# Optimization experiments

Hardware: AMD Instinct MI355X
Metric: run time of the kernel (lower is better)

The kernel has to match this reference:

```python
import jax, jax.numpy as jnp
import numpy as np

B, M, N, D = 16, 1024, 1024, 512
DIST_THRESH = 0.3
NUM_SINK = 8


def setup_inputs() -> dict:
    key = jax.random.key(0)
    k1, k2, k3, k4 = jax.random.split(key, 4)
    return {
        "tra_feats": jax.random.normal(k1, (B, M, D), jnp.float32),
        "det_feats": jax.random.normal(k2, (B, N, D), jnp.float32),
        "tra_loc": jax.random.uniform(k3, (B, M, 2), jnp.float32),
        "det_loc": jax.random.uniform(k4, (B, N, 2), jnp.float32),
        "alpha": jnp.ones((1,), jnp.float32),
        "eplison": jnp.zeros((1,), jnp.float32),
    }


def _sinkhorn(C, log_a, log_b, lambd, num_sink):
    # log-domain unrolled Sinkhorn: P_ij = exp(log_p), marginals a (rows), b (cols)
    log_p = -C / lambd
    def step(lp, _):
        lp = lp - (jax.nn.logsumexp(lp, axis=-1, keepdims=True) - log_a[:, None])
        lp = lp - (jax.nn.logsumexp(lp, axis=-2, keepdims=True) - log_b[None, :])
        return lp, None
    log_p, _ = jax.lax.scan(step, log_p, None, length=num_sink)
    # final row normalization (standard unrolled-sinkhorn convention)
    log_p = log_p - (jax.nn.logsumexp(log_p, axis=-1, keepdims=True) - log_a[:, None])
    return jnp.exp(log_p)


def _per_graph(tf, df, tl, dl, alpha, lambd):
    n1 = jnp.linalg.norm(tf, axis=-1, keepdims=True)          # [M,1]
    n2 = jnp.linalg.norm(df, axis=-1, keepdims=True)          # [N,1]
    d2 = jnp.sum((tl[:, None, :] - dl[None, :, :]) ** 2, -1)  # [M,N] squared cdist
    mask = (jnp.sqrt(d2) <= DIST_THRESH).astype(tf.dtype)
    corr = (tf @ df.T) / (n1 * n2.T) * mask                   # masked cosine similarity
    m, n = corr.shape
    # augment with dustbin row/col filled with learnable alpha
    top = jnp.concatenate([corr, jnp.full((m, 1), alpha, corr.dtype)], axis=1)
    bot = jnp.full((1, n + 1), alpha, corr.dtype)
    couplings = jnp.concatenate([top, bot], axis=0)           # [M+1, N+1]
    norm = 1.0 / (m + n)
    a_aug = jnp.full((m + 1,), norm, corr.dtype).at[-1].set(norm * n)
    b_aug = jnp.full((n + 1,), norm, corr.dtype).at[-1].set(norm * m)
    p = _sinkhorn(1.0 - couplings, jnp.log(a_aug), jnp.log(b_aug), lambd, NUM_SINK)
    return p * (m + n)


def reference(tra_feats, det_feats, tra_loc, det_loc, alpha, eplison):
    a = alpha[0]
    lambd = jnp.exp(eplison[0]) + 0.03
    f = jax.vmap(lambda tf, df, tl, dl: _per_graph(tf, df, tl, dl, a, lambd))
    return f(tra_feats, det_feats, tra_loc, det_loc)   # [B, M+1, N+1]
```

## Files before the change

### kernel.cpp

```cpp
#include <hip/hip_runtime.h>
#include <math.h>

#define B_ 16
#define M_ 1024
#define N_ 1024
#define D_ 512
#define MP1 1025
#define NP1 1025
#define NUM_SINK 8
#define BK 64
#define SSTR 1024
#define VSTR 1028
#define NCHK 16
#define LOG_NORM (-7.6246189861593985f)
#define LOG_HALF (-0.6931471805599453f)

typedef __attribute__((ext_vector_type(8))) short bf16x8;
typedef __attribute__((ext_vector_type(4))) float f32x4;
typedef __attribute__((ext_vector_type(8))) _Float16 h16x8;

__device__ inline short f2bf(float x) {
    unsigned u = __builtin_bit_cast(unsigned, x);
    u = (u + 0x7FFFu + ((u >> 16) & 1u)) >> 16;
    return (short)u;
}

__device__ inline void gload16(const void* g, void* l) {
    __builtin_amdgcn_global_load_lds(
        (const __attribute__((address_space(1))) unsigned int*)g,
        (__attribute__((address_space(3))) unsigned int*)l, 16, 0, 0);
}

template<bool PRE>
__global__ __launch_bounds__(256) void norms_kernel_t(
    const float* __restrict__ tf, const float* __restrict__ df,
    float* __restrict__ inv1, float* __restrict__ inv2,
    unsigned short* __restrict__ tfh, unsigned short* __restrict__ dfh,
    float* __restrict__ v, float* __restrict__ sums_p)
{
    if (PRE && blockIdx.x == 0) {
        const int nv = B_ * VSTR, ns = 2 * B_ * 17;
        for (int t = threadIdx.x; t < nv + ns; t += 256) {
            if (t < nv) v[t] = 0.f;
            else {
                int u2 = t - nv;
                int p = u2 / (B_ * 17), s = u2 % 17;
                sums_p[u2] = (p == 0 && s == 0) ? 1025.0f : 0.f;
            }
        }
    }
    int w = (blockIdx.x * 256 + threadIdx.x) >> 6;
    int lane = threadIdx.x & 63;
    if (w >= B_ * 2048) return;
    int b = w >> 11;
    int rr = w & 2047;
    const float* src;
    float* dst = nullptr;
    unsigned short* dsth = nullptr;
    if (rr < M_) { src = tf + ((size_t)b * M_ + rr) * D_;
                   if (!PRE) dst = inv1 + b * M_ + rr;
                   if (PRE)  dsth = tfh + ((size_t)b * M_ + rr) * D_; }
    else         { src = df + ((size_t)b * N_ + (rr - M_)) * D_;
                   if (!PRE) dst = inv2 + b * N_ + (rr - M_);
                   if (PRE)  dsth = dfh + ((size_t)b * N_ + (rr - M_)) * D_; }
    float4 x = *(const float4*)(src + lane * 4);
    float4 y = *(const float4*)(src + 256 + lane * 4);
    float ss = x.x*x.x + x.y*x.y + x.z*x.z + x.w*x.w
             + y.x*y.x + y.y*y.y + y.z*y.z + y.w*y.w;
    #pragma unroll
    for (int o = 32; o; o >>= 1) ss += __shfl_xor(ss, o);
    if (PRE) {
        float rn = rsqrtf(ss);
        ushort4 hx, hy;
        hx.x = (unsigned short)f2bf(x.x*rn); hx.y = (unsigned short)f2bf(x.y*rn);
        hx.z = (unsigned short)f2bf(x.z*rn); hx.w = (unsigned short)f2bf(x.w*rn);
        hy.x = (unsigned short)f2bf(y.x*rn); hy.y = (unsigned short)f2bf(y.y*rn);
        hy.z = (unsigned short)f2bf(y.z*rn); hy.w = (unsigned short)f2bf(y.w*rn);
        *(ushort4*)(dsth + lane * 4) = hx;
        *(ushort4*)(dsth + 256 + lane * 4) = hy;
    } else {
        if (lane == 0) *dst = 1.0f / sqrtf(ss);
    }
}

template<int MODE>
__global__ __launch_bounds__(256) void gemm_s_kernel(
    const void* __restrict__ A, const void* __restrict__ Bm,
    const float* __restrict__ tl, const float* __restrict__ dl,
    const float* __restrict__ inv1, const float* __restrict__ inv2,
    const float* __restrict__ eps_p, void* __restrict__ Sout)
{
    __shared__ __align__(16) unsigned short As[2][128 * BK];
    __shared__ __align__(16) unsigned short Bs[2][128 * BK];

    int flat = blockIdx.x;
    int swz = (flat & 7) * 128 + (flat >> 3);
    int jb = swz & 7, ib = (swz >> 3) & 7;
    int b  = swz >> 6;
    int i0 = ib * 128;
    int j0 = jb * 128;

    int tid  = threadIdx.x;
    int lane = tid & 63;
    int w    = tid >> 6;
    int wm   = w >> 1, wn = w & 1;

    f32x4 acc[4][4] = {};

    if constexpr (MODE == 2) {
        const unsigned short* Ah = (const unsigned short*)A  + (size_t)b * M_ * D_;
        const unsigned short* Bh = (const unsigned short*)Bm + (size_t)b * N_ * D_;
        int gcol = ((lane & 7) ^ (lane >> 3)) << 3;
        int rloc = lane >> 3;

        auto stage = [&](int k0, int buf) {
            #pragma unroll
            for (int c = 0; c < 4; ++c) {
                int r = (w * 4 + c) * 8 + rloc;
                gload16(Ah + (size_t)(i0 + r) * D_ + k0 + gcol,
                        (char*)As[buf] + (w * 4 + c) * 1024 + lane * 16);
                gload16(Bh + (size_t)(j0 + r) * D_ + k0 + gcol,
                        (char*)Bs[buf] + (w * 4 + c) * 1024 + lane * 16);
            }
        };

        stage(0, 0);
        __syncthreads();
        int cur = 0;
        for (int t = 0; t < D_ / BK; ++t) {
            if (t < D_ / BK - 1) stage((t + 1) * BK, cur ^ 1);
            #pragma unroll
            for (int ks = 0; ks < 2; ++ks) {
                int kb = ks * 64 + ((lane >> 4) << 4);
                bf16x8 af[4], bfr[4];
                #pragma unroll
                for (int m = 0; m < 4; ++m) {
                    int ra = wm * 64 + m * 16 + (lane & 15);
                    af[m] = *(const bf16x8*)((const char*)As[cur] + ra * 128 + (kb ^ ((ra & 7) << 4)));
                    int rb = wn * 64 + m * 16 + (lane & 15);
                    bfr[m] = *(const bf16x8*)((const char*)Bs[cur] + rb * 128 + (kb ^ ((rb & 7) << 4)));
                }
                #pragma unroll
                for (int m = 0; m < 4; ++m)
                    #pragma unroll
                    for (int n = 0; n < 4; ++n)
                        acc[m][n] = __builtin_amdgcn_mfma_f32_16x16x32_bf16(af[m], bfr[n], acc[m][n], 0, 0, 0);
            }
            __syncthreads();
            cur ^= 1;
        }
    } else {
        const float* Ab = (const float*)A  + (size_t)b * M_ * D_;
        const float* Bb = (const float*)Bm + (size_t)b * N_ * D_;
        int seg   = tid & 7;
        int rbase = tid >> 3;
        for (int k0 = 0; k0 < D_; k0 += BK) {
            #pragma unroll
            for (int rr = 0; rr < 4; ++rr) {
                int r = rbase + rr * 32;
                int colx = (seg * 16) ^ ((r & 7) << 4);
                {
                    const float* pa = Ab + (size_t)(i0 + r) * D_ + k0 + seg * 8;
                    float4 a0 = *(const float4*)pa;
                    float4 a1 = *(const float4*)(pa + 4);
                    bf16x8 hv;
                    hv[0] = f2bf(a0.x); hv[1] = f2bf(a0.y); hv[2] = f2bf(a0.z); hv[3] = f2bf(a0.w);
                    hv[4] = f2bf(a1.x); hv[5] = f2bf(a1.y); hv[6] = f2bf(a1.z); hv[7] = f2bf(a1.w);
                    *(bf16x8*)((char*)As[0] + r * 128 + colx) = hv;
                }
                {
                    const float* pb = Bb + (size_t)(j0 + r) * D_ + k0 + seg * 8;
                    float4 b0 = *(const float4*)pb;
                    float4 b1 = *(const float4*)(pb + 4);
                    bf16x8 hv;
                    hv[0] = f2bf(b0.x); hv[1] = f2bf(b0.y); hv[2] = f2bf(b0.z); hv[3] = f2bf(b0.w);
                    hv[4] = f2bf(b1.x); hv[5] = f2bf(b1.y); hv[6] = f2bf(b1.z); hv[7] = f2bf(b1.w);
                    *(bf16x8*)((char*)Bs[0] + r * 128 + colx) = hv;
                }
            }
            __syncthreads();
            #pragma unroll
            for (int ks = 0; ks < 2; ++ks) {
                int kb = ks * 64 + ((lane >> 4) << 4);
                bf16x8 af[4], bfr[4];
                #pragma unroll
                for (int m = 0; m < 4; ++m) {
                    int ra = wm * 64 + m * 16 + (lane & 15);
                    af[m] = *(const bf16x8*)((const char*)As[0] + ra * 128 + (kb ^ ((ra & 7) << 4)));
                    int rb = wn * 64 + m * 16 + (lane & 15);
                    bfr[m] = *(const bf16x8*)((const char*)Bs[0] + rb * 128 + (kb ^ ((rb & 7) << 4)));
                }
                #pragma unroll
                for (int m = 0; m < 4; ++m)
                    #pragma unroll
                    for (int n = 0; n < 4; ++n)
                        acc[m][n] = __builtin_amdgcn_mfma_f32_16x16x32_bf16(af[m], bfr[n], acc[m][n], 0, 0, 0);
            }
            __syncthreads();
        }
    }

    float lam = __expf(eps_p[0]) + 0.03f;
    float inv_lam = 1.0f / lam;
    int crow0 = i0 + wm * 64;
    int ccol0 = j0 + wn * 64;
    int rlane = lane >> 4;
    int clane = lane & 15;

    float invb_[4], dlx_[4], dly_[4];
    #pragma unroll
    for (int n = 0; n < 4; ++n) {
        int j = ccol0 + n * 16 + clane;
        if (MODE != 2) invb_[n] = inv2[b * N_ + j];
        dlx_[n]  = dl[((size_t)b * N_ + j) * 2 + 0];
        dly_[n]  = dl[((size_t)b * N_ + j) * 2 + 1];
    }
    #pragma unroll
    for (int m = 0; m < 4; ++m) {
        #pragma unroll
        for (int reg = 0; reg < 4; ++reg) {
            int i = crow0 + m * 16 + rlane * 4 + reg;
            float inva = (MODE != 2) ? inv1[b * M_ + i] : 1.0f;
            float tlx  = tl[((size_t)b * M_ + i) * 2 + 0];
            float tly  = tl[((size_t)b * M_ + i) * 2 + 1];
            #pragma unroll
            for (int n = 0; n < 4; ++n) {
                float cosv = (MODE == 2) ? acc[m][n][reg]
                                         : acc[m][n][reg] * inva * invb_[n];
                float dx = tlx - dlx_[n];
                float dy = tly - dly_[n];
                float mi = (fmaf(dx, dx, dy * dy) <= 0.09f) ? inv_lam : 0.0f;
                float val = fmaf(cosv, mi, -inv_lam);
                int col = ccol0 + n * 16 + clane;
                if (MODE >= 1) {
                    _Float16* Srow = (_Float16*)Sout + ((size_t)b * M_ + i) * SSTR;
                    Srow[col] = (_Float16)val;
                } else {
                    float* Srow = (float*)Sout + ((size_t)b * MP1 + i) * NP1;
                    Srow[col] = val;
                }
            }
        }
    }
}

__global__ __launch_bounds__(256) void init_hv(
    float* __restrict__ v, float* __restrict__ sums_p)
{
    int t = blockIdx.x * 256 + threadIdx.x;
    if (t < B_ * VSTR) v[t] = 0.f;
    int u2 = t - B_ * VSTR;
    if (u2 >= 0 && u2 < 2 * B_ * 17) {
        int p = u2 / (B_ * 17), s = u2 % 17;
        sums_p[u2] = (p == 0 && s == 0) ? 1025.0f : 0.f;
    }
}

__global__ __launch_bounds__(256, 1) void rowcol64(
    const _Float16* __restrict__ Sh, const float* __restrict__ v,
    float* __restrict__ ps,
    const float* __restrict__ alpha_p, const float* __restrict__ eps_p)
{
    int blk = blockIdx.x;
    int b = blk >> 4, k = blk & 15;
    int tid = threadIdx.x, lane = tid & 63, w = tid >> 6;

    __shared__ float red[4][64][17];

    const float* vb = v + (size_t)b * VSTR;
    float vreg[16];
    {
        float4 v0 = *(const float4*)(vb + lane * 8);
        float4 v1 = *(const float4*)(vb + lane * 8 + 4);
        float4 v2 = *(const float4*)(vb + 512 + lane * 8);
        float4 v3 = *(const float4*)(vb + 512 + lane * 8 + 4);
        vreg[0]=v0.x; vreg[1]=v0.y; vreg[2]=v0.z; vreg[3]=v0.w;
        vreg[4]=v1.x; vreg[5]=v1.y; vreg[6]=v1.z; vreg[7]=v1.w;
        vreg[8]=v2.x; vreg[9]=v2.y; vreg[10]=v2.z; vreg[11]=v2.w;
        vreg[12]=v3.x; vreg[13]=v3.y; vreg[14]=v3.z; vreg[15]=v3.w;
    }
    float lam = __expf(eps_p[0]) + 0.03f;
    float s_a = (alpha_p[0] - 1.0f) / lam;
    float et16c = __expf(s_a + vb[1024]);

    const _Float16* Sb = Sh + ((size_t)b << 20);
    int rbase = k * 64 + w * 16;

    h16x8 h0[16], h1[16];
    #pragma unroll
    for (int rr = 0; rr < 16; ++rr) {
        const _Float16* row = Sb + (size_t)(rbase + rr) * SSTR;
        h0[rr] = *(const h16x8*)(row + lane * 8);
        h1[rr] = *(const h16x8*)(row + 512 + lane * 8);
    }

    float creg[16] = {};
    float sum_scale = 0.f;

    #pragma unroll
    for (int rr = 0; rr < 16; ++rr) {
        float et[16];
        float rs = 0.f;
        #pragma unroll
        for (int e = 0; e < 8; ++e) { et[e] = __expf((float)h0[rr][e] + vreg[e]); rs += et[e]; }
        #pragma unroll
        for (int e = 0; e < 8; ++e) { et[8+e] = __expf((float)h1[rr][e] + vreg[8+e]); rs += et[8+e]; }
        #pragma unroll
        for (int o = 32; o; o >>= 1) rs += __shfl_xor(rs, o);
        rs += et16c;
        float scale = (1.0f / 2048.0f) / rs;
        #pragma unroll
        for (int e = 0; e < 16; ++e) creg[e] += et[e] * scale;
        sum_scale += scale;
    }

    #pragma unroll
    for (int e = 0; e < 16; ++e) red[w][lane][e] = creg[e];
    if (lane == 0) red[w][0][16] = sum_scale;
    __syncthreads();

    float* pso = ps + (size_t)(k * 16 + b) * 1025;
    for (int j = tid; j < 1024; j += 256) {
        int lane_j = (j & 511) >> 3;
        int e_j    = ((j >> 9) << 3) | (j & 7);
        pso[j] = red[0][lane_j][e_j] + red[1][lane_j][e_j]
               + red[2][lane_j][e_j] + red[3][lane_j][e_j];
    }
    if (tid == 0)
        pso[1024] = et16c * (red[0][0][16] + red[1][0][16] + red[2][0][16] + red[3][0][16]);
}

__global__ __launch_bounds__(256) void colpass32(
    const float* __restrict__ ps, float* __restrict__ v,
    float* __restrict__ sums_p, int it)
{
    int gw = blockIdx.x * 4 + (threadIdx.x >> 6);
    int lane = threadIdx.x & 63;
    if (gw >= B_ * 17) return;
    int b = gw / 17, seg = gw % 17;
    int j = seg * 64 + lane;
    int par = it & 1;
    float sum_old = 0.f;
    #pragma unroll
    for (int s = 0; s < 17; ++s) sum_old += sums_p[par * (B_ * 17) + b * 17 + s];
    float ev = 0.f;
    if (j <= 1024) {
        size_t vidx = (size_t)b * VSTR + j;
        float vj = v[vidx];
        const float* pp = ps + (size_t)b * 1025 + j;
        float cs = 0.f;
        #pragma unroll
        for (int c = 0; c < NCHK; ++c) cs += pp[(size_t)c * (16 * 1025)];
        cs += 0.5f * __expf(vj) / sum_old;
        float lb = (j == 1024) ? LOG_HALF : LOG_NORM;
        float vn = vj + lb - __logf(cs);
        v[vidx] = vn;
        ev = __expf(vn);
    }
    #pragma unroll
    for (int o = 32; o; o >>= 1) ev += __shfl_xor(ev, o);
    if (lane == 0) sums_p[(par ^ 1) * (B_ * 17) + b * 17 + seg] = ev;
}

__global__ __launch_bounds__(256) void final32(
    const _Float16* __restrict__ Sh, const float* __restrict__ v,
    const float* __restrict__ sums_p,
    const float* __restrict__ alpha_p, const float* __restrict__ eps_p,
    float* __restrict__ out)
{
    int blk = blockIdx.x;
    int tid = threadIdx.x, lane = tid & 63, w = tid >> 6;

    if (blk >= 512) {
        int gw = (blk - 512) * 4 + w;
        if (gw >= B_ * 17) return;
        int b = gw / 17, seg = gw % 17, j = seg * 64 + lane;
        if (j > 1024) return;
        float sumv = 0.f;
        int par = NUM_SINK & 1;
        #pragma unroll
        for (int s = 0; s < 17; ++s) sumv += sums_p[par * (B_ * 17) + b * 17 + s];
        out[((size_t)b * MP1 + 1024) * NP1 + j] = __expf(v[(size_t)b * VSTR + j]) * 1024.0f / sumv;
        return;
    }

    int b = blk >> 5, k = blk & 31;
    const float* vb = v + (size_t)b * VSTR;
    float vreg[16];
    {
        float4 v0 = *(const float4*)(vb + lane * 8);
        float4 v1 = *(const float4*)(vb + lane * 8 + 4);
        float4 v2 = *(const float4*)(vb + 512 + lane * 8);
        float4 v3 = *(const float4*)(vb + 512 + lane * 8 + 4);
        vreg[0]=v0.x; vreg[1]=v0.y; vreg[2]=v0.z; vreg[3]=v0.w;
        vreg[4]=v1.x; vreg[5]=v1.y; vreg[6]=v1.z; vreg[7]=v1.w;
        vreg[8]=v2.x; vreg[9]=v2.y; vreg[10]=v2.z; vreg[11]=v2.w;
        vreg[12]=v3.x; vreg[13]=v3.y; vreg[14]=v3.z; vreg[15]=v3.w;
    }
    float lam = __expf(eps_p[0]) + 0.03f;
    float s_a = (alpha_p[0] - 1.0f) / lam;
    float et16c = __expf(s_a + vb[1024]);

    const _Float16* Sb = Sh + ((size_t)b << 20);
    int rbase = k * 32 + w * 8;

    #pragma unroll
    for (int g = 0; g < 2; ++g) {
        h16x8 h0[4], h1[4];
        #pragma unroll
        for (int rr = 0; rr < 4; ++rr) {
            const _Float16* row = Sb + (size_t)(rbase + g * 4 + rr) * SSTR;
            h0[rr] = *(const h16x8*)(row + lane * 8);
            h1[rr] = *(const h16x8*)(row + 512 + lane * 8);
        }
        #pragma unroll
        for (int rr = 0; rr < 4; ++rr) {
            int r = rbase + g * 4 + rr;
            float et[16];
            float rs = 0.f;
            #pragma unroll
            for (int e = 0; e < 8; ++e) { et[e] = __expf((float)h0[rr][e] + vreg[e]); rs += et[e]; }
            #pragma unroll
            for (int e = 0; e < 8; ++e) { et[8+e] = __expf((float)h1[rr][e] + vreg[8+e]); rs += et[8+e]; }
            #pragma unroll
            for (int o = 32; o; o >>= 1) rs += __shfl_xor(rs, o);
            rs += et16c;
            float sc = 1.0f / rs;
            float* orow = out + ((size_t)b * MP1 + r) * NP1;
            float4 o0 = {et[0]*sc,  et[1]*sc,  et[2]*sc,  et[3]*sc};
            float4 o1 = {et[4]*sc,  et[5]*sc,  et[6]*sc,  et[7]*sc};
            float4 o2 = {et[8]*sc,  et[9]*sc,  et[10]*sc, et[11]*sc};
            float4 o3 = {et[12]*sc, et[13]*sc, et[14]*sc, et[15]*sc};
            *(float4*)(orow + lane * 8)           = o0;
            *(float4*)(orow + lane * 8 + 4)       = o1;
            *(float4*)(orow + 512 + lane * 8)     = o2;
            *(float4*)(orow + 512 + lane * 8 + 4) = o3;
            if (lane == 0) orow[1024] = et16c * sc;
        }
    }
}


__global__ __launch_bounds__(256) void fill_edges_f32(
    float* __restrict__ Sout, const float* __restrict__ alpha_p, const float* __restrict__ eps_p)
{
    int t = blockIdx.x * 256 + threadIdx.x;
    if (t >= B_ * (NP1 + M_)) return;
    int b = t / (NP1 + M_), r = t % (NP1 + M_);
    float lam = expf(eps_p[0]) + 0.03f;
    float s = (alpha_p[0] - 1.0f) / lam;
    size_t idx;
    if (r < NP1) idx = ((size_t)b * MP1 + M_) * NP1 + r;
    else         idx = ((size_t)b * MP1 + (r - NP1)) * NP1 + N_;
    Sout[idx] = s;
}

__global__ __launch_bounds__(256) void row_pass_kernel(
    const float* __restrict__ S, const float* __restrict__ v, float* __restrict__ u)
{
    int w = (blockIdx.x * 256 + threadIdx.x) >> 6;
    int lane = threadIdx.x & 63;
    if (w >= B_ * MP1) return;
    int b = w / MP1, i = w % MP1;
    const float* row = S + ((size_t)b * MP1 + i) * NP1;
    const float* vb = v + b * NP1;
    float sm = 0.f;
    #pragma unroll
    for (int q = 0; q < 17; ++q) {
        int j = lane + q * 64;
        if (j < NP1) sm += expf(row[j] + vb[j]);
    }
    #pragma unroll
    for (int o = 32; o; o >>= 1) sm += __shfl_xor(sm, o);
    if (lane == 0) {
        float la = (i == M_) ? LOG_HALF : LOG_NORM;
        u[b * MP1 + i] = la - logf(sm);
    }
}

__global__ __launch_bounds__(256) void col_pass1_kernel(
    const float* __restrict__ S, const float* __restrict__ u,
    float* __restrict__ pm, float* __restrict__ ps)
{
    int j = blockIdx.x * 256 + threadIdx.x;
    int b = blockIdx.z;
    int i0 = blockIdx.y * 128;
    int i1 = min(i0 + 128, MP1);
    if (j >= NP1) return;
    const float* p  = S + ((size_t)b * MP1 + i0) * NP1 + j;
    const float* ub = u + b * MP1;
    float sm = 0.f;
    for (int i = i0; i < i1; ++i) {
        sm += expf(*p + ub[i]);
        p += NP1;
    }
    int idx = (blockIdx.y * B_ + b) * NP1 + j;
    pm[idx] = 0.f;
    ps[idx] = sm;
}

__global__ __launch_bounds__(256) void col_pass2_kernel(
    const float* __restrict__ pm, const float* __restrict__ ps, float* __restrict__ v)
{
    int j = blockIdx.x * 256 + threadIdx.x;
    int b = blockIdx.y;
    if (j >= NP1) return;
    float Ssum = 0.f;
    #pragma unroll
    for (int c = 0; c < 9; ++c) Ssum += ps[(c * B_ + b) * NP1 + j];
    float lb = (j == N_) ? LOG_HALF : LOG_NORM;
    v[b * NP1 + j] = lb - logf(Ssum);
}

__global__ __launch_bounds__(256) void row_final_kernel(
    float* __restrict__ S, const float* __restrict__ v)
{
    int w = (blockIdx.x * 256 + threadIdx.x) >> 6;
    int lane = threadIdx.x & 63;
    if (w >= B_ * MP1) return;
    int b = w / MP1, i = w % MP1;
    float* row = S + ((size_t)b * MP1 + i) * NP1;
    const float* vb = v + b * NP1;
    float et[17];
    float sm = 0.f;
    #pragma unroll
    for (int q = 0; q < 17; ++q) {
        int j = lane + q * 64;
        float e = 0.f;
        if (j < NP1) e = expf(row[j] + vb[j]);
        et[q] = e;
        sm += e;
    }
    #pragma unroll
    for (int o = 32; o; o >>= 1) sm += __shfl_xor(sm, o);
    float A = (i == M_) ? 0.5f : (1.0f / 2048.0f);
    float scale = (A / sm) * 2048.0f;
    #pragma unroll
    for (int q = 0; q < 17; ++q) {
        int j = lane + q * 64;
        if (j < NP1) row[j] = et[q] * scale;
    }
}

__global__ __launch_bounds__(256) void zero_kernel(float* __restrict__ p, int n)
{
    int i = blockIdx.x * 256 + threadIdx.x;
    if (i < n) p[i] = 0.f;
}

extern "C" void kernel_launch(void* const* d_in, const int* in_sizes, int n_in,
                              void* d_out, int out_size, void* d_ws, size_t ws_size,
                              hipStream_t stream)
{
    const float* tf    = (const float*)d_in[0];
    const float* df    = (const float*)d_in[1];
    const float* tl    = (const float*)d_in[2];
    const float* dl    = (const float*)d_in[3];
    const float* alpha = (const float*)d_in[4];
    const float* eps   = (const float*)d_in[5];
    float* out = (float*)d_out;

    const size_t bf_one   = (size_t)B_ * M_ * D_ * 2;
    const size_t sh_bytes = (size_t)B_ * M_ * SSTR * 2;
    const size_t vf       = (size_t)B_ * VSTR;
    const size_t sums_f   = 2 * B_ * 17;
    const size_t invs_f   = (size_t)B_ * M_ * 2;
    const size_t need_pre = 2 * bf_one + sh_bytes + (vf + sums_f) * 4 + 512;
    const size_t need_mid = sh_bytes + (vf + sums_f + invs_f) * 4 + 512;

    int initblocks = (int)((vf + sums_f + 255) / 256);

    if (ws_size >= need_pre) {
        unsigned short* tfh = (unsigned short*)d_ws;
        unsigned short* dfh = tfh + (size_t)B_ * M_ * D_;
        _Float16* Sh = (_Float16*)((char*)d_ws + 2 * bf_one);
        float* fbase = (float*)((char*)d_ws + ((2 * bf_one + sh_bytes + 255) & ~(size_t)255));
        float* v      = fbase;
        float* sums_p = v + vf;
        float* ps     = out;

        norms_kernel_t<true><<<(B_ * 2048) / 4, 256, 0, stream>>>(tf, df, nullptr, nullptr, tfh, dfh, v, sums_p);
        gemm_s_kernel<2><<<1024, 256, 0, stream>>>(tfh, dfh, tl, dl, nullptr, nullptr, eps, Sh);

        for (int it = 0; it < NUM_SINK; ++it) {
            rowcol64<<<256, 256, 0, stream>>>(Sh, v, ps, alpha, eps);
            colpass32<<<68, 256, 0, stream>>>(ps, v, sums_p, it);
        }
        final32<<<580, 256, 0, stream>>>(Sh, v, sums_p, alpha, eps, out);
    } else if (ws_size >= need_mid) {
        _Float16* Sh = (_Float16*)d_ws;
        float* fbase = (float*)((char*)d_ws + ((sh_bytes + 255) & ~(size_t)255));
        float* inv1   = fbase;
        float* inv2   = inv1 + B_ * M_;
        float* v      = inv2 + B_ * N_;
        float* sums_p = v + vf;
        float* ps     = out;

        init_hv<<<initblocks, 256, 0, stream>>>(v, sums_p);
        norms_kernel_t<false><<<(B_ * 2048) / 4, 256, 0, stream>>>(tf, df, inv1, inv2, nullptr, nullptr, nullptr, nullptr);
        gemm_s_kernel<1><<<1024, 256, 0, stream>>>(tf, df, tl, dl, inv1, inv2, eps, Sh);

        for (int it = 0; it < NUM_SINK; ++it) {
            rowcol64<<<256, 256, 0, stream>>>(Sh, v, ps, alpha, eps);
            colpass32<<<68, 256, 0, stream>>>(ps, v, sums_p, it);
        }
        final32<<<580, 256, 0, stream>>>(Sh, v, sums_p, alpha, eps, out);
    } else {
        float* S = out;
        float* ws = (float*)d_ws;
        float* inv1 = ws;
        float* inv2 = inv1 + B_ * M_;
        float* u    = inv2 + B_ * N_;
        float* v    = u + B_ * MP1;
        float* pm   = v + B_ * NP1;
        float* ps   = pm + 9 * B_ * NP1;

        zero_kernel<<<(B_ * NP1 + 255) / 256, 256, 0, stream>>>(v, B_ * NP1);
        norms_kernel_t<false><<<(B_ * 2048) / 4, 256, 0, stream>>>(tf, df, inv1, inv2, nullptr, nullptr, nullptr, nullptr);
        gemm_s_kernel<0><<<1024, 256, 0, stream>>>(tf, df, tl, dl, inv1, inv2, eps, S);
        fill_edges_f32<<<(B_ * (NP1 + M_) + 255) / 256, 256, 0, stream>>>(S, alpha, eps);

        int rowblocks = (B_ * MP1 + 3) / 4;
        for (int it = 0; it < NUM_SINK; ++it) {
            row_pass_kernel<<<rowblocks, 256, 0, stream>>>(S, v, u);
            col_pass1_kernel<<<dim3(5, 9, 16), 256, 0, stream>>>(S, u, pm, ps);
            col_pass2_kernel<<<dim3(5, 16), 256, 0, stream>>>(pm, ps, v);
        }
        row_final_kernel<<<rowblocks, 256, 0, stream>>>(S, v);
    }
}
```

Before: 150.9 us.

## Fuse column-update pass into row kernel with ping-pong v and partial-sum buffers

Removes the separate colpass32 launch per Sinkhorn iteration. Each rowcolv64 block now recomputes the column potential v for its batch redundantly from the previous iteration's partial sums, using double-buffered v and ps arrays indexed by iteration parity. Initialisation of v is handled by an it==0 branch instead of a separate init step. The aim is to cut 8 launches and their inter-kernel gaps. The cost is redundant per-block column reductions (16 blocks per batch each read 16x1025 partials) and a larger workspace.

New measurement: 168.8 us. 11.9% more time.

```diff
diff --git a/kernel.cpp b/kernel.cpp
--- a/kernel.cpp
+++ b/kernel.cpp
@@ -12,6 +12,7 @@
 #define SSTR 1024
 #define VSTR 1028
 #define NCHK 16
+#define PSTOT (16 * B_ * 1025)
 #define LOG_NORM (-7.6246189861593985f)
 #define LOG_HALF (-0.6931471805599453f)
 
@@ -35,20 +36,8 @@
 __global__ __launch_bounds__(256) void norms_kernel_t(
     const float* __restrict__ tf, const float* __restrict__ df,
     float* __restrict__ inv1, float* __restrict__ inv2,
-    unsigned short* __restrict__ tfh, unsigned short* __restrict__ dfh,
-    float* __restrict__ v, float* __restrict__ sums_p)
-{
-    if (PRE && blockIdx.x == 0) {
-        const int nv = B_ * VSTR, ns = 2 * B_ * 17;
-        for (int t = threadIdx.x; t < nv + ns; t += 256) {
-            if (t < nv) v[t] = 0.f;
-            else {
-                int u2 = t - nv;
-                int p = u2 / (B_ * 17), s = u2 % 17;
-                sums_p[u2] = (p == 0 && s == 0) ? 1025.0f : 0.f;
-            }
-        }
-    }
+    unsigned short* __restrict__ tfh, unsigned short* __restrict__ dfh)
+{
     int w = (blockIdx.x * 256 + threadIdx.x) >> 6;
     int lane = threadIdx.x & 63;
     if (w >= B_ * 2048) return;
@@ -244,44 +233,19 @@
     }
 }
 
-__global__ __launch_bounds__(256) void init_hv(
-    float* __restrict__ v, float* __restrict__ sums_p)
-{
-    int t = blockIdx.x * 256 + threadIdx.x;
-    if (t < B_ * VSTR) v[t] = 0.f;
-    int u2 = t - B_ * VSTR;
-    if (u2 >= 0 && u2 < 2 * B_ * 17) {
-        int p = u2 / (B_ * 17), s = u2 % 17;
-        sums_p[u2] = (p == 0 && s == 0) ? 1025.0f : 0.f;
-    }
-}
-
-__global__ __launch_bounds__(256, 1) void rowcol64(
-    const _Float16* __restrict__ Sh, const float* __restrict__ v,
-    float* __restrict__ ps,
-    const float* __restrict__ alpha_p, const float* __restrict__ eps_p)
+__global__ __launch_bounds__(256, 1) void rowcolv64(
+    const _Float16* __restrict__ Sh, float* __restrict__ vbuf,
+    float* __restrict__ psbuf,
+    const float* __restrict__ alpha_p, const float* __restrict__ eps_p,
+    int it)
 {
     int blk = blockIdx.x;
     int b = blk >> 4, k = blk & 15;
     int tid = threadIdx.x, lane = tid & 63, w = tid >> 6;
 
     __shared__ float red[4][64][17];
-
-    const float* vb = v + (size_t)b * VSTR;
-    float vreg[16];
-    {
-        float4 v0 = *(const float4*)(vb + lane * 8);
-        float4 v1 = *(const float4*)(vb + lane * 8 + 4);
-        float4 v2 = *(const float4*)(vb + 512 + lane * 8);
-        float4 v3 = *(const float4*)(vb + 512 + lane * 8 + 4);
-        vreg[0]=v0.x; vreg[1]=v0.y; vreg[2]=v0.z; vreg[3]=v0.w;
-        vreg[4]=v1.x; vreg[5]=v1.y; vreg[6]=v1.z; vreg[7]=v1.w;
-        vreg[8]=v2.x; vreg[9]=v2.y; vreg[10]=v2.z; vreg[11]=v2.w;
-        vreg[12]=v3.x; vreg[13]=v3.y; vreg[14]=v3.z; vreg[15]=v3.w;
-    }
-    float lam = __expf(eps_p[0]) + 0.03f;
-    float s_a = (alpha_p[0] - 1.0f) / lam;
-    float et16c = __expf(s_a + vb[1024]);
+    __shared__ float vsh[1025];
+    __shared__ float wred[4];
 
     const _Float16* Sb = Sh + ((size_t)b << 20);
     int rbase = k * 64 + w * 16;
@@ -294,6 +258,57 @@
         h1[rr] = *(const h16x8*)(row + 512 + lane * 8);
     }
 
+    int rp = it & 1, wp = rp ^ 1;
+
+    if (it == 0) {
+        for (int j = tid; j < 1025; j += 256) vsh[j] = 0.f;
+    } else {
+        const float* vin = vbuf + (size_t)rp * (B_ * VSTR) + (size_t)b * VSTR;
+        const float* pin = psbuf + (size_t)rp * PSTOT + (size_t)b * 1025;
+        float vp[4]; float vp4 = 0.f;
+        float evs = 0.f;
+        #pragma unroll
+        for (int q = 0; q < 4; ++q) { vp[q] = vin[tid + q * 256]; evs += __expf(vp[q]); }
+        if (tid == 0) { vp4 = vin[1024]; evs += __expf(vp4); }
+        #pragma unroll
+        for (int o = 32; o; o >>= 1) evs += __shfl_xor(evs, o);
+        if (lane == 0) wred[w] = evs;
+        __syncthreads();
+        float Sev = wred[0] + wred[1] + wred[2] + wred[3];
+        #pragma unroll
+        for (int q = 0; q < 4; ++q) {
+            int j = tid + q * 256;
+            float cs = 0.f;
+            #pragma unroll
+            for (int c = 0; c < NCHK; ++c) cs += pin[(size_t)c * (B_ * 1025) + j];
+            cs += 0.5f * __expf(vp[q]) / Sev;
+            vsh[j] = vp[q] + LOG_NORM - __logf(cs);
+        }
+        if (tid == 0) {
+            float cs = 0.f;
+            #pragma unroll
+            for (int c = 0; c < NCHK; ++c) cs += pin[(size_t)c * (B_ * 1025) + 1024];
+            cs += 0.5f * __expf(vp4) / Sev;
+            vsh[1024] = vp4 + LOG_HALF - __logf(cs);
+        }
+    }
+    __syncthreads();
+
+    if (k == 0) {
+        float* vout = vbuf + (size_t)wp * (B_ * VSTR) + (size_t)b * VSTR;
+        for (int j = tid; j < 1025; j += 256) vout[j] = vsh[j];
+    }
+
+    float vreg[16];
+    #pragma unroll
+    for (int e = 0; e < 8; ++e) {
+        vreg[e]     = vsh[lane * 8 + e];
+        vreg[8 + e] = vsh[512 + lane * 8 + e];
+    }
+    float lam = __expf(eps_p[0]) + 0.03f;
+    float s_a = (alpha_p[0] - 1.0f) / lam;
+    float et16c = __expf(s_a + vsh[1024]);
+
     float creg[16] = {};
     float sum_scale = 0.f;
 
@@ -319,7 +334,7 @@
     if (lane == 0) red[w][0][16] = sum_scale;
     __syncthreads();
 
-    float* pso = ps + (size_t)(k * 16 + b) * 1025;
+    float* pso = psbuf + (size_t)wp * PSTOT + (size_t)(k * B_ + b) * 1025;
     for (int j = tid; j < 1024; j += 256) {
         int lane_j = (j & 511) >> 3;
         int e_j    = ((j >> 9) << 3) | (j & 7);
@@ -330,76 +345,77 @@
         pso[1024] = et16c * (red[0][0][16] + red[1][0][16] + red[2][0][16] + red[3][0][16]);
 }
 
-__global__ __launch_bounds__(256) void colpass32(
-    const float* __restrict__ ps, float* __restrict__ v,
-    float* __restrict__ sums_p, int it)
-{
-    int gw = blockIdx.x * 4 + (threadIdx.x >> 6);
-    int lane = threadIdx.x & 63;
-    if (gw >= B_ * 17) return;
-    int b = gw / 17, seg = gw % 17;
-    int j = seg * 64 + lane;
-    int par = it & 1;
-    float sum_old = 0.f;
-    #pragma unroll
-    for (int s = 0; s < 17; ++s) sum_old += sums_p[par * (B_ * 17) + b * 17 + s];
-    float ev = 0.f;
-    if (j <= 1024) {
-        size_t vidx = (size_t)b * VSTR + j;
-        float vj = v[vidx];
-        const float* pp = ps + (size_t)b * 1025 + j;
-        float cs = 0.f;
-        #pragma unroll
-        for (int c = 0; c < NCHK; ++c) cs += pp[(size_t)c * (16 * 1025)];
-        cs += 0.5f * __expf(vj) / sum_old;
-        float lb = (j == 1024) ? LOG_HALF : LOG_NORM;
-        float vn = vj + lb - __logf(cs);
-        v[vidx] = vn;
-        ev = __expf(vn);
-    }
-    #pragma unroll
-    for (int o = 32; o; o >>= 1) ev += __shfl_xor(ev, o);
-    if (lane == 0) sums_p[(par ^ 1) * (B_ * 17) + b * 17 + seg] = ev;
-}
-
-__global__ __launch_bounds__(256) void final32(
-    const _Float16* __restrict__ Sh, const float* __restrict__ v,
-    const float* __restrict__ sums_p,
+__global__ __launch_bounds__(256) void finalv(
+    const _Float16* __restrict__ Sh, const float* __restrict__ vbuf,
+    const float* __restrict__ psbuf,
     const float* __restrict__ alpha_p, const float* __restrict__ eps_p,
     float* __restrict__ out)
 {
     int blk = blockIdx.x;
+    bool dust = blk >= 512;
+    int b = dust ? (blk - 512) : (blk >> 5);
+    int k = blk & 31;
     int tid = threadIdx.x, lane = tid & 63, w = tid >> 6;
 
-    if (blk >= 512) {
-        int gw = (blk - 512) * 4 + w;
-        if (gw >= B_ * 17) return;
-        int b = gw / 17, seg = gw % 17, j = seg * 64 + lane;
-        if (j > 1024) return;
-        float sumv = 0.f;
-        int par = NUM_SINK & 1;
-        #pragma unroll
-        for (int s = 0; s < 17; ++s) sumv += sums_p[par * (B_ * 17) + b * 17 + s];
-        out[((size_t)b * MP1 + 1024) * NP1 + j] = __expf(v[(size_t)b * VSTR + j]) * 1024.0f / sumv;
+    __shared__ float vsh[1025];
+    __shared__ float wred[4];
+
+    const int rp = NUM_SINK & 1;
+    {
+        const float* vin = vbuf + (size_t)rp * (B_ * VSTR) + (size_t)b * VSTR;
+        const float* pin = psbuf + (size_t)rp * PSTOT + (size_t)b * 1025;
+        float vp[4]; float vp4 = 0.f;
+        float evs = 0.f;
+        #pragma unroll
+        for (int q = 0; q < 4; ++q) { vp[q] = vin[tid + q * 256]; evs += __expf(vp[q]); }
+        if (tid == 0) { vp4 = vin[1024]; evs += __expf(vp4); }
+        #pragma unroll
+        for (int o = 32; o; o >>= 1) evs += __shfl_xor(evs, o);
+        if (lane == 0) wred[w] = evs;
+        __syncthreads();
+        float Sev = wred[0] + wred[1] + wred[2] + wred[3];
+        #pragma unroll
+        for (int q = 0; q < 4; ++q) {
+            int j = tid + q * 256;
+            float cs = 0.f;
+            #pragma unroll
+            for (int c = 0; c < NCHK; ++c) cs += pin[(size_t)c * (B_ * 1025) + j];
+            cs += 0.5f * __expf(vp[q]) / Sev;
+            vsh[j] = vp[q] + LOG_NORM - __logf(cs);
+        }
+        if (tid == 0) {
+            float cs = 0.f;
+            #pragma unroll
+            for (int c = 0; c < NCHK; ++c) cs += pin[(size_t)c * (B_ * 1025) + 1024];
+            cs += 0.5f * __expf(vp4) / Sev;
+            vsh[1024] = vp4 + LOG_HALF - __logf(cs);
+        }
+    }
+    __syncthreads();
+
+    if (dust) {
+        float evs = 0.f;
+        for (int j = tid; j < 1025; j += 256) evs += __expf(vsh[j]);
+        #pragma unroll
+        for (int o = 32; o; o >>= 1) evs += __shfl_xor(evs, o);
+        if (lane == 0) wred[w] = evs;
+        __syncthreads();
+        float Sev8 = wred[0] + wred[1] + wred[2] + wred[3];
+        float* orow = out + ((size_t)b * MP1 + 1024) * NP1;
+        for (int j = tid; j < 1025; j += 256)
+            orow[j] = __expf(vsh[j]) * 1024.0f / Sev8;
         return;
     }
 
-    int b = blk >> 5, k = blk & 31;
-    const float* vb = v + (size_t)b * VSTR;
     float vreg[16];
-    {
-        float4 v0 = *(const float4*)(vb + lane * 8);
-        float4 v1 = *(const float4*)(vb + lane * 8 + 4);
-        float4 v2 = *(const float4*)(vb + 512 + lane * 8);
-        float4 v3 = *(const float4*)(vb + 512 + lane * 8 + 4);
-        vreg[0]=v0.x; vreg[1]=v0.y; vreg[2]=v0.z; vreg[3]=v0.w;
-        vreg[4]=v1.x; vreg[5]=v1.y; vreg[6]=v1.z; vreg[7]=v1.w;
-        vreg[8]=v2.x; vreg[9]=v2.y; vreg[10]=v2.z; vreg[11]=v2.w;
-        vreg[12]=v3.x; vreg[13]=v3.y; vreg[14]=v3.z; vreg[15]=v3.w;
+    #pragma unroll
+    for (int e = 0; e < 8; ++e) {
+        vreg[e]     = vsh[lane * 8 + e];
+        vreg[8 + e] = vsh[512 + lane * 8 + e];
     }
     float lam = __expf(eps_p[0]) + 0.03f;
     float s_a = (alpha_p[0] - 1.0f) / lam;
-    float et16c = __expf(s_a + vb[1024]);
+    float et16c = __expf(s_a + vsh[1024]);
 
     const _Float16* Sb = Sh + ((size_t)b << 20);
     int rbase = k * 32 + w * 8;
@@ -562,49 +578,40 @@
 
     const size_t bf_one   = (size_t)B_ * M_ * D_ * 2;
     const size_t sh_bytes = (size_t)B_ * M_ * SSTR * 2;
-    const size_t vf       = (size_t)B_ * VSTR;
-    const size_t sums_f   = 2 * B_ * 17;
+    const size_t vf2      = 2 * (size_t)B_ * VSTR;
+    const size_t ps2      = 2 * (size_t)PSTOT;
     const size_t invs_f   = (size_t)B_ * M_ * 2;
-    const size_t need_pre = 2 * bf_one + sh_bytes + (vf + sums_f) * 4 + 512;
-    const size_t need_mid = sh_bytes + (vf + sums_f + invs_f) * 4 + 512;
-
-    int initblocks = (int)((vf + sums_f + 255) / 256);
+    const size_t need_pre = 2 * bf_one + sh_bytes + (vf2 + ps2) * 4 + 512;
+    const size_t need_mid = sh_bytes + (vf2 + ps2 + invs_f) * 4 + 512;
 
     if (ws_size >= need_pre) {
         unsigned short* tfh = (unsigned short*)d_ws;
         unsigned short* dfh = tfh + (size_t)B_ * M_ * D_;
         _Float16* Sh = (_Float16*)((char*)d_ws + 2 * bf_one);
         float* fbase = (float*)((char*)d_ws + ((2 * bf_one + sh_bytes + 255) & ~(size_t)255));
-        float* v      = fbase;
-        float* sums_p = v + vf;
-        float* ps     = out;
-
-        norms_kernel_t<true><<<(B_ * 2048) / 4, 256, 0, stream>>>(tf, df, nullptr, nullptr, tfh, dfh, v, sums_p);
+        float* vbuf  = fbase;
+        float* psbuf = vbuf + vf2;
+
+        norms_kernel_t<true><<<(B_ * 2048) / 4, 256, 0, stream>>>(tf, df, nullptr, nullptr, tfh, dfh);
         gemm_s_kernel<2><<<1024, 256, 0, stream>>>(tfh, dfh, tl, dl, nullptr, nullptr, eps, Sh);
 
-        for (int it = 0; it < NUM_SINK; ++it) {
-            rowcol64<<<256, 256, 0, stream>>>(Sh, v, ps, alpha, eps);
-            colpass32<<<68, 256, 0, stream>>>(ps, v, sums_p, it);
-        }
-        final32<<<580, 256, 0, stream>>>(Sh, v, sums_p, alpha, eps, out);
+        for (int it = 0; it < NUM_SINK; ++it)
+            rowcolv64<<<256, 256, 0, stream>>>(Sh, vbuf, psbuf, alpha, eps, it);
+        finalv<<<512 + B_, 256, 0, stream>>>(Sh, vbuf, psbuf, alpha, eps, out);
     } else if (ws_size >= need_mid) {
         _Float16* Sh = (_Float16*)d_ws;
         float* fbase = (float*)((char*)d_ws + ((sh_bytes + 255) & ~(size_t)255));
-        float* inv1   = fbase;
-        float* inv2   = inv1 + B_ * M_;
-        float* v      = inv2 + B_ * N_;
-        float* sums_p = v + vf;
-        float* ps     = out;
-
-        init_hv<<<initblocks, 256, 0, stream>>>(v, sums_p);
-        norms_kernel_t<false><<<(B_ * 2048) / 4, 256, 0, stream>>>(tf, df, inv1, inv2, nullptr, nullptr, nullptr, nullptr);
+        float* inv1  = fbase;
+        float* inv2  = inv1 + B_ * M_;
+        float* vbuf  = inv2 + B_ * N_;
+        float* psbuf = vbuf + vf2;
+
+        norms_kernel_t<false><<<(B_ * 2048) / 4, 256, 0, stream>>>(tf, df, inv1, inv2, nullptr, nullptr);
         gemm_s_kernel<1><<<1024, 256, 0, stream>>>(tf, df, tl, dl, inv1, inv2, eps, Sh);
 
-        for (int it = 0; it < NUM_SINK; ++it) {
-            rowcol64<<<256, 256, 0, stream>>>(Sh, v, ps, alpha, eps);
-            colpass32<<<68, 256, 0, stream>>>(ps, v, sums_p, it);
-        }
-        final32<<<580, 256, 0, stream>>>(Sh, v, sums_p, alpha, eps, out);
+        for (int it = 0; it < NUM_SINK; ++it)
+            rowcolv64<<<256, 256, 0, stream>>>(Sh, vbuf, psbuf, alpha, eps, it);
+        finalv<<<512 + B_, 256, 0, stream>>>(Sh, vbuf, psbuf, alpha, eps, out);
     } else {
         float* S = out;
         float* ws = (float*)d_ws;
@@ -616,7 +623,7 @@
         float* ps   = pm + 9 * B_ * NP1;
 
         zero_kernel<<<(B_ * NP1 + 255) / 256, 256, 0, stream>>>(v, B_ * NP1);
-        norms_kernel_t<false><<<(B_ * 2048) / 4, 256, 0, stream>>>(tf, df, inv1, inv2, nullptr, nullptr, nullptr, nullptr);
+        norms_kernel_t<false><<<(B_ * 2048) / 4, 256, 0, stream>>>(tf, df, inv1, inv2, nullptr, nullptr);
         gemm_s_kernel<0><<<1024, 256, 0, stream>>>(tf, df, tl, dl, inv1, inv2, eps, S);
         fill_edges_f32<<<(B_ * (NP1 + M_) + 255) / 256, 256, 0, stream>>>(S, alpha, eps);
 
```
